# Kernel optimization log

Hardware: AMD Instinct MI355X
Metric: run time of the kernel (lower is better)

Reference implementation:

```python
import jax, jax.numpy as jnp
import numpy as np
from jax import lax

R = 128          # residual channels
DILATION = 4


def setup_inputs() -> dict:
    key = jax.random.key(0)
    ks = jax.random.split(key, 9)
    B, Cin, T = 8, 128, 16000
    Ccond, S, K = 80, 256, 3
    s = 0.05
    return {
        "input": jax.random.normal(ks[0], (B, Cin, T), dtype=jnp.float32),
        "cond_input": jax.random.normal(ks[1], (B, Ccond, T), dtype=jnp.float32),
        "weight_conv": jax.random.normal(ks[2], (2 * R, Cin, K), dtype=jnp.float32) * s,
        "bias_conv": jax.random.normal(ks[3], (2 * R,), dtype=jnp.float32) * s,
        "weight_cond": jax.random.normal(ks[4], (2 * R, Ccond, 1), dtype=jnp.float32) * s,
        "weight_out": jax.random.normal(ks[5], (R, R, 1), dtype=jnp.float32) * s,
        "bias_out": jax.random.normal(ks[6], (R,), dtype=jnp.float32) * s,
        "weight_skip": jax.random.normal(ks[7], (S, R, 1), dtype=jnp.float32) * s,
        "bias_skip": jax.random.normal(ks[8], (S,), dtype=jnp.float32) * s,
    }


def reference(input, cond_input, weight_conv, bias_conv, weight_cond,
              weight_out, bias_out, weight_skip, bias_skip):
    # Causal dilated Conv1d: left-pad (K-1)*dilation
    K = weight_conv.shape[-1]
    pad = (K - 1) * DILATION
    x = lax.conv_general_dilated(
        input, weight_conv, window_strides=(1,),
        padding=[(pad, 0)], rhs_dilation=(DILATION,),
        dimension_numbers=("NCH", "OIH", "NCH"))  # (B, 2R, T)
    x = x + bias_conv[None, :, None]
    # cond_1x1 (kernel 1, no bias), added to pre-activation
    x = x + jnp.einsum("bct,oc->bot", cond_input, weight_cond[:, :, 0])
    # gated activation: tanh(first half) * sigmoid(second half)
    z = jnp.tanh(x[:, :R, :]) * jax.nn.sigmoid(x[:, R:, :])  # (B, R, T)
    skip = jnp.einsum("bct,oc->bot", z, weight_skip[:, :, 0]) + bias_skip[None, :, None]
    output = jnp.einsum("bct,oc->bot", z, weight_out[:, :, 0]) + bias_out[None, :, None]
    return (output, skip)
```

## Files before the change

### kernel.cpp

```cpp
#include <hip/hip_runtime.h>


#define NB 8
#define NT 16000
#define CIN 128
#define CCOND 80
#define CCP 96
#define TT 128
#define NROW 136

typedef __attribute__((ext_vector_type(8))) __bf16 bf16x8;
typedef __attribute__((ext_vector_type(4))) float f32x4;
typedef __attribute__((ext_vector_type(4))) unsigned short u16x4;
typedef __attribute__((ext_vector_type(4))) unsigned int u32x4;

__device__ __forceinline__ unsigned short f2bf(float f) {
  unsigned int u = __float_as_uint(f);
  return (unsigned short)((u + 0x7fffu + ((u >> 16) & 1u)) >> 16);
}
__device__ __forceinline__ bf16x8 ldb8(const unsigned short* p) {
  return *reinterpret_cast<const bf16x8*>(p);
}

__global__ void pack_weights(const float* __restrict__ wc, const float* __restrict__ wcd,
                             const float* __restrict__ wo, const float* __restrict__ wsk,
                             unsigned short* __restrict__ wpc,
                             unsigned short* __restrict__ wpcd,
                             unsigned short* __restrict__ wp2)
{
  int idx = blockIdx.x * 256 + threadIdx.x;
  if (idx < 98304) {
    int o = idx / 384, k = idx - o * 384;
    int tap = k >> 7, c = k & 127;
    wpc[idx] = f2bf(wc[(o * 128 + c) * 3 + tap]);
  } else if (idx < 122880) {
    int i = idx - 98304;
    int o = i / 96, k = i - o * 96;
    wpcd[i] = f2bf(k < CCOND ? wcd[o * CCOND + k] : 0.f);
  } else if (idx < 172032) {
    int i = idx - 122880;
    int m = i >> 7, k = i & 127;
    wp2[i] = f2bf(m < 128 ? wo[m * 128 + k] : wsk[(m - 128) * 128 + k]);
  }
}

__global__ __launch_bounds__(512, 4) void k12_fused(
    const unsigned short* __restrict__ wpc, const unsigned short* __restrict__ wpcd,
    const unsigned short* __restrict__ wp2,
    const float* __restrict__ in, const float* __restrict__ cond,
    const float* __restrict__ bconv, const float* __restrict__ bout,
    const float* __restrict__ bskip, float* __restrict__ out)
{
  __shared__ u32x4 ldsX_[2176];
  __shared__ u32x4 ldsU_[2048];
  char* ldsX = (char*)ldsX_;
  char* ldsU = (char*)ldsU_;

  int b = blockIdx.y;
  int t0 = blockIdx.x * TT;
  int tid = threadIdx.x;
  int lane = tid & 63, w = tid >> 6;
  int l15 = lane & 15, g = lane >> 4;

  #pragma unroll
  for (int rep = 0; rep < 5; ++rep) {
    int gi = rep * 512 + tid;
    if (gi < 16 * NROW) {
      int gch = gi / NROW;
      int row = gi - gch * NROW;
      int t = t0 - 8 + row;
      u32x4 pk = {};
      if (t >= 0) {
        const float* src = &in[((size_t)b * CIN + gch * 8) * NT + t];
        #pragma unroll
        for (int p = 0; p < 4; ++p) {
          float v0 = src[(size_t)(2 * p) * NT];
          float v1 = src[(size_t)(2 * p + 1) * NT];
          pk[p] = (unsigned)f2bf(v0) | ((unsigned)f2bf(v1) << 16);
        }
      }
      *reinterpret_cast<u32x4*>(&ldsX[row * 256 + ((gch ^ (row & 7)) << 4)]) = pk;
    }
  }
  #pragma unroll
  for (int rep = 0; rep < 3; ++rep) {
    int gi = rep * 512 + tid;
    int gch = gi >> 7;
    int row = gi & 127;
    u32x4 pk = {};
    if (gch < 10) {
      const float* src = &cond[((size_t)b * CCOND + gch * 8) * NT + t0 + row];
      #pragma unroll
      for (int p = 0; p < 4; ++p) {
        float v0 = src[(size_t)(2 * p) * NT];
        float v1 = src[(size_t)(2 * p + 1) * NT];
        pk[p] = (unsigned)f2bf(v0) | ((unsigned)f2bf(v1) << 16);
      }
    }
    *reinterpret_cast<u32x4*>(&ldsU[row * 192 + ((gch ^ (row & 3)) << 4)]) = pk;
  }
  __syncthreads();

  int rt = 16 * w + l15, rs = 128 + 16 * w + l15;
  f32x4 at[8] = {}, as_[8] = {};

  #pragma unroll
  for (int gg = 0; gg < 5; ++gg) {
    bf16x8 wt[3], wss[3];
    #pragma unroll
    for (int q = 0; q < 3; ++q) {
      int s = gg * 3 + q;
      if (s < 12) {
        int tap = s >> 2, kc = s & 3;
        wt[q]  = ldb8(&wpc[(size_t)rt * 384 + tap * 128 + kc * 32 + g * 8]);
        wss[q] = ldb8(&wpc[(size_t)rs * 384 + tap * 128 + kc * 32 + g * 8]);
      } else {
        int kc = s - 12;
        wt[q]  = ldb8(&wpcd[(size_t)rt * CCP + kc * 32 + g * 8]);
        wss[q] = ldb8(&wpcd[(size_t)rs * CCP + kc * 32 + g * 8]);
      }
    }
    __builtin_amdgcn_sched_barrier(0);
    #pragma unroll
    for (int q = 0; q < 3; ++q) {
      int s = gg * 3 + q;
      if (s < 12) {
        int tap = s >> 2, kc = s & 3;
        int ck = kc * 4 + g;
        #pragma unroll
        for (int nf = 0; nf < 8; ++nf) {
          int tl = nf * 16 + l15 + tap * 4;
          bf16x8 bfr = *reinterpret_cast<const bf16x8*>(&ldsX[tl * 256 + ((ck ^ (tl & 7)) << 4)]);
          at[nf]  = __builtin_amdgcn_mfma_f32_16x16x32_bf16(wt[q],  bfr, at[nf],  0, 0, 0);
          as_[nf] = __builtin_amdgcn_mfma_f32_16x16x32_bf16(wss[q], bfr, as_[nf], 0, 0, 0);
        }
      } else {
        int kc = s - 12;
        int ck = kc * 4 + g;
        #pragma unroll
        for (int nf = 0; nf < 8; ++nf) {
          int r = nf * 16 + l15;
          bf16x8 bfr = *reinterpret_cast<const bf16x8*>(&ldsU[r * 192 + ((ck ^ (r & 3)) << 4)]);
          at[nf]  = __builtin_amdgcn_mfma_f32_16x16x32_bf16(wt[q],  bfr, at[nf],  0, 0, 0);
          as_[nf] = __builtin_amdgcn_mfma_f32_16x16x32_bf16(wss[q], bfr, as_[nf], 0, 0, 0);
        }
      }
    }
  }

  float btv[4], bsv[4];
  #pragma unroll
  for (int j = 0; j < 4; ++j) {
    btv[j] = bconv[16 * w + g * 4 + j];
    bsv[j] = bconv[128 + 16 * w + g * 4 + j];
  }

  bf16x8 wk2buf[2][4];
  #pragma unroll
  for (int kc = 0; kc < 4; ++kc)
    wk2buf[0][kc] = ldb8(&wp2[(size_t)(48 * w + l15) * 128 + kc * 32 + g * 8]);

  __syncthreads();

  {
    int cg = 2 * w + (g >> 1);
    int off = (g & 1) * 8;
    #pragma unroll
    for (int nf = 0; nf < 8; ++nf) {
      int tl = nf * 16 + l15;
      u16x4 pk;
      #pragma unroll
      for (int j = 0; j < 4; ++j) {
        float a = at[nf][j] + btv[j];
        float s = as_[nf][j] + bsv[j];
        float z = (1.f - 2.f / (1.f + __expf(2.f * a))) * (1.f / (1.f + __expf(-s)));
        pk[j] = f2bf(z);
      }
      *reinterpret_cast<u16x4*>(&ldsU[tl * 256 + ((cg ^ (tl & 7)) << 4) + off]) = pk;
    }
  }
  __syncthreads();

  float* skipp = out + (size_t)NB * 128 * NT;
  #pragma unroll
  for (int mf = 0; mf < 3; ++mf) {
    bf16x8* wcur = wk2buf[mf & 1];
    bf16x8* wnx  = wk2buf[(mf + 1) & 1];
    if (mf < 2) {
      #pragma unroll
      for (int kc = 0; kc < 4; ++kc)
        wnx[kc] = ldb8(&wp2[(size_t)(48 * w + 16 * (mf + 1) + l15) * 128 + kc * 32 + g * 8]);
    }
    __builtin_amdgcn_sched_barrier(0);
    f32x4 am[8] = {};
    #pragma unroll
    for (int kc = 0; kc < 4; ++kc) {
      #pragma unroll
      for (int nf = 0; nf < 8; ++nf) {
        int r = nf * 16 + l15;
        bf16x8 bfr = *reinterpret_cast<const bf16x8*>(&ldsU[r * 256 + (((kc * 4 + g) ^ (r & 7)) << 4)]);
        am[nf] = __builtin_amdgcn_mfma_f32_16x16x32_bf16(wcur[kc], bfr, am[nf], 0, 0, 0);
      }
    }
    int mrow = 48 * w + 16 * mf + g * 4;
    #pragma unroll
    for (int j = 0; j < 4; ++j) {
      int m = mrow + j;
      float bv;
      float* basep;
      if (m < 128) { bv = bout[m];        basep = out   + ((size_t)b * 128 + m) * NT; }
      else         { bv = bskip[m - 128]; basep = skipp + ((size_t)b * 256 + (m - 128)) * NT; }
      #pragma unroll
      for (int nf = 0; nf < 8; ++nf)
        basep[t0 + nf * 16 + l15] = am[nf][j] + bv;
    }
  }
}

extern "C" void kernel_launch(void* const* d_in, const int* in_sizes, int n_in,
                              void* d_out, int out_size, void* d_ws, size_t ws_size,
                              hipStream_t stream)
{
  const float* input = (const float*)d_in[0];
  const float* cond  = (const float*)d_in[1];
  const float* wconv = (const float*)d_in[2];
  const float* bconv = (const float*)d_in[3];
  const float* wcond = (const float*)d_in[4];
  const float* wout  = (const float*)d_in[5];
  const float* boutp = (const float*)d_in[6];
  const float* wskip = (const float*)d_in[7];
  const float* bskip = (const float*)d_in[8];
  float* out = (float*)d_out;

  unsigned short* wpc  = (unsigned short*)d_ws;
  unsigned short* wpcd = wpc + 98304;
  unsigned short* wp2  = wpcd + 24576;

  pack_weights<<<672, 256, 0, stream>>>(wconv, wcond, wout, wskip, wpc, wpcd, wp2);
  k12_fused<<<dim3(NT / TT, NB), 512, 0, stream>>>(wpc, wpcd, wp2, input, cond,
                                                   bconv, boutp, bskip, out);
}
```

Measured before the change: 106.4 us.

## Overlap cond loads with conv MFMAs, use hardware bf16 pack, restructure output GEMM

The input tile is now staged first, followed by a barrier. The cond tile global loads are then issued before the conv-tap MFMAs so they can overlap, and the cond GEMM runs after a second barrier. Float-to-bf16 conversion switches from manual integer rounding to the v_cvt_pk_bf16_f32 instruction. The second GEMM is reorganised into two time halves, each computing all three M fragments with B fragments reused across them, and the weight double-buffer and sched_barriers are dropped. This trades register pressure and an extra barrier for better latency hiding and fewer VALU ops.

```diff
diff --git a/kernel.cpp b/kernel.cpp
--- a/kernel.cpp
+++ b/kernel.cpp
@@ -11,12 +11,17 @@
 
 typedef __attribute__((ext_vector_type(8))) __bf16 bf16x8;
 typedef __attribute__((ext_vector_type(4))) float f32x4;
-typedef __attribute__((ext_vector_type(4))) unsigned short u16x4;
+typedef __attribute__((ext_vector_type(2))) unsigned int u32x2;
 typedef __attribute__((ext_vector_type(4))) unsigned int u32x4;
 
 __device__ __forceinline__ unsigned short f2bf(float f) {
   unsigned int u = __float_as_uint(f);
   return (unsigned short)((u + 0x7fffu + ((u >> 16) & 1u)) >> 16);
+}
+__device__ __forceinline__ unsigned cvtpk(float lo, float hi) {
+  unsigned r;
+  asm("v_cvt_pk_bf16_f32 %0, %1, %2" : "=v"(r) : "v"(lo), "v"(hi));
+  return r;
 }
 __device__ __forceinline__ bf16x8 ldb8(const unsigned short* p) {
   return *reinterpret_cast<const bf16x8*>(p);
@@ -73,15 +78,14 @@
       if (t >= 0) {
         const float* src = &in[((size_t)b * CIN + gch * 8) * NT + t];
         #pragma unroll
-        for (int p = 0; p < 4; ++p) {
-          float v0 = src[(size_t)(2 * p) * NT];
-          float v1 = src[(size_t)(2 * p + 1) * NT];
-          pk[p] = (unsigned)f2bf(v0) | ((unsigned)f2bf(v1) << 16);
-        }
+        for (int p = 0; p < 4; ++p)
+          pk[p] = cvtpk(src[(size_t)(2 * p) * NT], src[(size_t)(2 * p + 1) * NT]);
       }
       *reinterpret_cast<u32x4*>(&ldsX[row * 256 + ((gch ^ (row & 7)) << 4)]) = pk;
     }
   }
+  __syncthreads();
+
   #pragma unroll
   for (int rep = 0; rep < 3; ++rep) {
     int gi = rep * 512 + tid;
@@ -91,59 +95,57 @@
     if (gch < 10) {
       const float* src = &cond[((size_t)b * CCOND + gch * 8) * NT + t0 + row];
       #pragma unroll
-      for (int p = 0; p < 4; ++p) {
-        float v0 = src[(size_t)(2 * p) * NT];
-        float v1 = src[(size_t)(2 * p + 1) * NT];
-        pk[p] = (unsigned)f2bf(v0) | ((unsigned)f2bf(v1) << 16);
-      }
+      for (int p = 0; p < 4; ++p)
+        pk[p] = cvtpk(src[(size_t)(2 * p) * NT], src[(size_t)(2 * p + 1) * NT]);
     }
     *reinterpret_cast<u32x4*>(&ldsU[row * 192 + ((gch ^ (row & 3)) << 4)]) = pk;
   }
-  __syncthreads();
 
   int rt = 16 * w + l15, rs = 128 + 16 * w + l15;
   f32x4 at[8] = {}, as_[8] = {};
 
   #pragma unroll
-  for (int gg = 0; gg < 5; ++gg) {
+  for (int gg = 0; gg < 4; ++gg) {
     bf16x8 wt[3], wss[3];
     #pragma unroll
     for (int q = 0; q < 3; ++q) {
       int s = gg * 3 + q;
-      if (s < 12) {
-        int tap = s >> 2, kc = s & 3;
-        wt[q]  = ldb8(&wpc[(size_t)rt * 384 + tap * 128 + kc * 32 + g * 8]);
-        wss[q] = ldb8(&wpc[(size_t)rs * 384 + tap * 128 + kc * 32 + g * 8]);
-      } else {
-        int kc = s - 12;
-        wt[q]  = ldb8(&wpcd[(size_t)rt * CCP + kc * 32 + g * 8]);
-        wss[q] = ldb8(&wpcd[(size_t)rs * CCP + kc * 32 + g * 8]);
-      }
-    }
-    __builtin_amdgcn_sched_barrier(0);
+      int tap = s >> 2, kc = s & 3;
+      wt[q]  = ldb8(&wpc[(size_t)rt * 384 + tap * 128 + kc * 32 + g * 8]);
+      wss[q] = ldb8(&wpc[(size_t)rs * 384 + tap * 128 + kc * 32 + g * 8]);
+    }
     #pragma unroll
     for (int q = 0; q < 3; ++q) {
       int s = gg * 3 + q;
-      if (s < 12) {
-        int tap = s >> 2, kc = s & 3;
-        int ck = kc * 4 + g;
-        #pragma unroll
-        for (int nf = 0; nf < 8; ++nf) {
-          int tl = nf * 16 + l15 + tap * 4;
-          bf16x8 bfr = *reinterpret_cast<const bf16x8*>(&ldsX[tl * 256 + ((ck ^ (tl & 7)) << 4)]);
-          at[nf]  = __builtin_amdgcn_mfma_f32_16x16x32_bf16(wt[q],  bfr, at[nf],  0, 0, 0);
-          as_[nf] = __builtin_amdgcn_mfma_f32_16x16x32_bf16(wss[q], bfr, as_[nf], 0, 0, 0);
-        }
-      } else {
-        int kc = s - 12;
-        int ck = kc * 4 + g;
-        #pragma unroll
-        for (int nf = 0; nf < 8; ++nf) {
-          int r = nf * 16 + l15;
-          bf16x8 bfr = *reinterpret_cast<const bf16x8*>(&ldsU[r * 192 + ((ck ^ (r & 3)) << 4)]);
-          at[nf]  = __builtin_amdgcn_mfma_f32_16x16x32_bf16(wt[q],  bfr, at[nf],  0, 0, 0);
-          as_[nf] = __builtin_amdgcn_mfma_f32_16x16x32_bf16(wss[q], bfr, as_[nf], 0, 0, 0);
-        }
+      int tap = s >> 2, kc = s & 3;
+      int ck = kc * 4 + g;
+      #pragma unroll
+      for (int nf = 0; nf < 8; ++nf) {
+        int tl = nf * 16 + l15 + tap * 4;
+        bf16x8 bfr = *reinterpret_cast<const bf16x8*>(&ldsX[tl * 256 + ((ck ^ (tl & 7)) << 4)]);
+        at[nf]  = __builtin_amdgcn_mfma_f32_16x16x32_bf16(wt[q],  bfr, at[nf],  0, 0, 0);
+        as_[nf] = __builtin_amdgcn_mfma_f32_16x16x32_bf16(wss[q], bfr, as_[nf], 0, 0, 0);
+      }
+    }
+  }
+  __syncthreads();
+
+  {
+    bf16x8 wt[3], wss[3];
+    #pragma unroll
+    for (int kc = 0; kc < 3; ++kc) {
+      wt[kc]  = ldb8(&wpcd[(size_t)rt * CCP + kc * 32 + g * 8]);
+      wss[kc] = ldb8(&wpcd[(size_t)rs * CCP + kc * 32 + g * 8]);
+    }
+    #pragma unroll
+    for (int kc = 0; kc < 3; ++kc) {
+      int ck = kc * 4 + g;
+      #pragma unroll
+      for (int nf = 0; nf < 8; ++nf) {
+        int r = nf * 16 + l15;
+        bf16x8 bfr = *reinterpret_cast<const bf16x8*>(&ldsU[r * 192 + ((ck ^ (r & 3)) << 4)]);
+        at[nf]  = __builtin_amdgcn_mfma_f32_16x16x32_bf16(wt[kc],  bfr, at[nf],  0, 0, 0);
+        as_[nf] = __builtin_amdgcn_mfma_f32_16x16x32_bf16(wss[kc], bfr, as_[nf], 0, 0, 0);
       }
     }
   }
@@ -154,12 +156,6 @@
     btv[j] = bconv[16 * w + g * 4 + j];
     bsv[j] = bconv[128 + 16 * w + g * 4 + j];
   }
-
-  bf16x8 wk2buf[2][4];
-  #pragma unroll
-  for (int kc = 0; kc < 4; ++kc)
-    wk2buf[0][kc] = ldb8(&wp2[(size_t)(48 * w + l15) * 128 + kc * 32 + g * 8]);
-
   __syncthreads();
 
   {
@@ -168,51 +164,57 @@
     #pragma unroll
     for (int nf = 0; nf < 8; ++nf) {
       int tl = nf * 16 + l15;
-      u16x4 pk;
+      float zv[4];
       #pragma unroll
       for (int j = 0; j < 4; ++j) {
         float a = at[nf][j] + btv[j];
         float s = as_[nf][j] + bsv[j];
-        float z = (1.f - 2.f / (1.f + __expf(2.f * a))) * (1.f / (1.f + __expf(-s)));
-        pk[j] = f2bf(z);
-      }
-      *reinterpret_cast<u16x4*>(&ldsU[tl * 256 + ((cg ^ (tl & 7)) << 4) + off]) = pk;
+        zv[j] = (1.f - 2.f / (1.f + __expf(2.f * a))) * (1.f / (1.f + __expf(-s)));
+      }
+      u32x2 pk;
+      pk[0] = cvtpk(zv[0], zv[1]);
+      pk[1] = cvtpk(zv[2], zv[3]);
+      *reinterpret_cast<u32x2*>(&ldsU[tl * 256 + ((cg ^ (tl & 7)) << 4) + off]) = pk;
     }
   }
   __syncthreads();
 
   float* skipp = out + (size_t)NB * 128 * NT;
   #pragma unroll
-  for (int mf = 0; mf < 3; ++mf) {
-    bf16x8* wcur = wk2buf[mf & 1];
-    bf16x8* wnx  = wk2buf[(mf + 1) & 1];
-    if (mf < 2) {
-      #pragma unroll
-      for (int kc = 0; kc < 4; ++kc)
-        wnx[kc] = ldb8(&wp2[(size_t)(48 * w + 16 * (mf + 1) + l15) * 128 + kc * 32 + g * 8]);
-    }
-    __builtin_amdgcn_sched_barrier(0);
-    f32x4 am[8] = {};
+  for (int half = 0; half < 2; ++half) {
+    f32x4 acc2[3][4] = {};
     #pragma unroll
     for (int kc = 0; kc < 4; ++kc) {
-      #pragma unroll
-      for (int nf = 0; nf < 8; ++nf) {
-        int r = nf * 16 + l15;
-        bf16x8 bfr = *reinterpret_cast<const bf16x8*>(&ldsU[r * 256 + (((kc * 4 + g) ^ (r & 7)) << 4)]);
-        am[nf] = __builtin_amdgcn_mfma_f32_16x16x32_bf16(wcur[kc], bfr, am[nf], 0, 0, 0);
-      }
-    }
-    int mrow = 48 * w + 16 * mf + g * 4;
-    #pragma unroll
-    for (int j = 0; j < 4; ++j) {
-      int m = mrow + j;
-      float bv;
-      float* basep;
-      if (m < 128) { bv = bout[m];        basep = out   + ((size_t)b * 128 + m) * NT; }
-      else         { bv = bskip[m - 128]; basep = skipp + ((size_t)b * 256 + (m - 128)) * NT; }
-      #pragma unroll
-      for (int nf = 0; nf < 8; ++nf)
-        basep[t0 + nf * 16 + l15] = am[nf][j] + bv;
+      bf16x8 w2[3];
+      #pragma unroll
+      for (int mf = 0; mf < 3; ++mf)
+        w2[mf] = ldb8(&wp2[(size_t)(48 * w + 16 * mf + l15) * 128 + kc * 32 + g * 8]);
+      bf16x8 bfr[4];
+      #pragma unroll
+      for (int nf = 0; nf < 4; ++nf) {
+        int r = (half * 4 + nf) * 16 + l15;
+        bfr[nf] = *reinterpret_cast<const bf16x8*>(&ldsU[r * 256 + (((kc * 4 + g) ^ (r & 7)) << 4)]);
+      }
+      #pragma unroll
+      for (int mf = 0; mf < 3; ++mf)
+        #pragma unroll
+        for (int nf = 0; nf < 4; ++nf)
+          acc2[mf][nf] = __builtin_amdgcn_mfma_f32_16x16x32_bf16(w2[mf], bfr[nf], acc2[mf][nf], 0, 0, 0);
+    }
+    #pragma unroll
+    for (int mf = 0; mf < 3; ++mf) {
+      int mrow = 48 * w + 16 * mf + g * 4;
+      #pragma unroll
+      for (int j = 0; j < 4; ++j) {
+        int m = mrow + j;
+        float bv;
+        float* basep;
+        if (m < 128) { bv = bout[m];        basep = out   + ((size_t)b * 128 + m) * NT; }
+        else         { bv = bskip[m - 128]; basep = skipp + ((size_t)b * 256 + (m - 128)) * NT; }
+        #pragma unroll
+        for (int nf = 0; nf < 4; ++nf)
+          basep[t0 + (half * 4 + nf) * 16 + l15] = acc2[mf][nf][j] + bv;
+      }
     }
   }
 }
```

After: 121.1 us. 13.9% more time.

## Shrink time tile to 112 and switch LDS to channel-major layout

Applied to the files above, without the earlier changes.

Reduces the per-block time tile from 128 to 112 columns, which gives 143 blocks per batch with bounds checks for the ragged tail, and replaces the XOR-swizzled row-major LDS layout with a channel-group-major layout using padded strides. The gated activation is written back into the input LDS buffer rather than a separate one, so shared memory per block drops and more blocks can be resident or the grid fills the CUs more evenly. The risk is LDS bank conflicts from the new unswizzled strides, extra boundary branches, and a smaller MFMA N-tile per wave.

```diff
diff --git a/kernel.cpp b/kernel.cpp
--- a/kernel.cpp
+++ b/kernel.cpp
@@ -5,9 +5,11 @@
 #define NT 16000
 #define CIN 128
 #define CCOND 80
-#define CCP 96
-#define TT 128
-#define NROW 136
+#define TT 112
+#define XR 120
+#define XSTRIDE 1920
+#define CSTRIDE 1792
+#define NBLK 143
 
 typedef __attribute__((ext_vector_type(8))) __bf16 bf16x8;
 typedef __attribute__((ext_vector_type(4))) float f32x4;
@@ -51,10 +53,10 @@
     const float* __restrict__ bconv, const float* __restrict__ bout,
     const float* __restrict__ bskip, float* __restrict__ out)
 {
-  __shared__ u32x4 ldsX_[2176];
-  __shared__ u32x4 ldsU_[2048];
+  __shared__ u32x4 ldsX_[XR * 16];
+  __shared__ u32x4 ldsC_[112 * 10];
   char* ldsX = (char*)ldsX_;
-  char* ldsU = (char*)ldsU_;
+  char* ldsC = (char*)ldsC_;
 
   int b = blockIdx.y;
   int t0 = blockIdx.x * TT;
@@ -63,14 +65,14 @@
   int l15 = lane & 15, g = lane >> 4;
 
   #pragma unroll
-  for (int rep = 0; rep < 5; ++rep) {
+  for (int rep = 0; rep < 4; ++rep) {
     int gi = rep * 512 + tid;
-    if (gi < 16 * NROW) {
-      int gch = gi / NROW;
-      int row = gi - gch * NROW;
+    if (gi < 16 * XR) {
+      int gch = gi / XR;
+      int row = gi - gch * XR;
       int t = t0 - 8 + row;
       u32x4 pk = {};
-      if (t >= 0) {
+      if (t >= 0 && t < NT) {
         const float* src = &in[((size_t)b * CIN + gch * 8) * NT + t];
         #pragma unroll
         for (int p = 0; p < 4; ++p) {
@@ -79,30 +81,33 @@
           pk[p] = (unsigned)f2bf(v0) | ((unsigned)f2bf(v1) << 16);
         }
       }
-      *reinterpret_cast<u32x4*>(&ldsX[row * 256 + ((gch ^ (row & 7)) << 4)]) = pk;
+      *reinterpret_cast<u32x4*>(&ldsX[gch * XSTRIDE + row * 16]) = pk;
     }
   }
   #pragma unroll
   for (int rep = 0; rep < 3; ++rep) {
     int gi = rep * 512 + tid;
-    int gch = gi >> 7;
-    int row = gi & 127;
-    u32x4 pk = {};
-    if (gch < 10) {
-      const float* src = &cond[((size_t)b * CCOND + gch * 8) * NT + t0 + row];
-      #pragma unroll
-      for (int p = 0; p < 4; ++p) {
-        float v0 = src[(size_t)(2 * p) * NT];
-        float v1 = src[(size_t)(2 * p + 1) * NT];
-        pk[p] = (unsigned)f2bf(v0) | ((unsigned)f2bf(v1) << 16);
-      }
-    }
-    *reinterpret_cast<u32x4*>(&ldsU[row * 192 + ((gch ^ (row & 3)) << 4)]) = pk;
+    if (gi < 10 * TT) {
+      int gch = gi / TT;
+      int row = gi - gch * TT;
+      int t = t0 + row;
+      u32x4 pk = {};
+      if (t < NT) {
+        const float* src = &cond[((size_t)b * CCOND + gch * 8) * NT + t];
+        #pragma unroll
+        for (int p = 0; p < 4; ++p) {
+          float v0 = src[(size_t)(2 * p) * NT];
+          float v1 = src[(size_t)(2 * p + 1) * NT];
+          pk[p] = (unsigned)f2bf(v0) | ((unsigned)f2bf(v1) << 16);
+        }
+      }
+      *reinterpret_cast<u32x4*>(&ldsC[gch * CSTRIDE + row * 16]) = pk;
+    }
   }
   __syncthreads();
 
   int rt = 16 * w + l15, rs = 128 + 16 * w + l15;
-  f32x4 at[8] = {}, as_[8] = {};
+  f32x4 at[7] = {}, as_[7] = {};
 
   #pragma unroll
   for (int gg = 0; gg < 5; ++gg) {
@@ -116,8 +121,8 @@
         wss[q] = ldb8(&wpc[(size_t)rs * 384 + tap * 128 + kc * 32 + g * 8]);
       } else {
         int kc = s - 12;
-        wt[q]  = ldb8(&wpcd[(size_t)rt * CCP + kc * 32 + g * 8]);
-        wss[q] = ldb8(&wpcd[(size_t)rs * CCP + kc * 32 + g * 8]);
+        wt[q]  = ldb8(&wpcd[(size_t)rt * 96 + kc * 32 + g * 8]);
+        wss[q] = ldb8(&wpcd[(size_t)rs * 96 + kc * 32 + g * 8]);
       }
     }
     __builtin_amdgcn_sched_barrier(0);
@@ -128,9 +133,9 @@
         int tap = s >> 2, kc = s & 3;
         int ck = kc * 4 + g;
         #pragma unroll
-        for (int nf = 0; nf < 8; ++nf) {
-          int tl = nf * 16 + l15 + tap * 4;
-          bf16x8 bfr = *reinterpret_cast<const bf16x8*>(&ldsX[tl * 256 + ((ck ^ (tl & 7)) << 4)]);
+        for (int nf = 0; nf < 7; ++nf) {
+          int row = nf * 16 + l15 + tap * 4;
+          bf16x8 bfr = *reinterpret_cast<const bf16x8*>(&ldsX[ck * XSTRIDE + row * 16]);
           at[nf]  = __builtin_amdgcn_mfma_f32_16x16x32_bf16(wt[q],  bfr, at[nf],  0, 0, 0);
           as_[nf] = __builtin_amdgcn_mfma_f32_16x16x32_bf16(wss[q], bfr, as_[nf], 0, 0, 0);
         }
@@ -138,9 +143,10 @@
         int kc = s - 12;
         int ck = kc * 4 + g;
         #pragma unroll
-        for (int nf = 0; nf < 8; ++nf) {
+        for (int nf = 0; nf < 7; ++nf) {
           int r = nf * 16 + l15;
-          bf16x8 bfr = *reinterpret_cast<const bf16x8*>(&ldsU[r * 192 + ((ck ^ (r & 3)) << 4)]);
+          bf16x8 bfr = {};
+          if (ck < 10) bfr = *reinterpret_cast<const bf16x8*>(&ldsC[ck * CSTRIDE + r * 16]);
           at[nf]  = __builtin_amdgcn_mfma_f32_16x16x32_bf16(wt[q],  bfr, at[nf],  0, 0, 0);
           as_[nf] = __builtin_amdgcn_mfma_f32_16x16x32_bf16(wss[q], bfr, as_[nf], 0, 0, 0);
         }
@@ -166,7 +172,7 @@
     int cg = 2 * w + (g >> 1);
     int off = (g & 1) * 8;
     #pragma unroll
-    for (int nf = 0; nf < 8; ++nf) {
+    for (int nf = 0; nf < 7; ++nf) {
       int tl = nf * 16 + l15;
       u16x4 pk;
       #pragma unroll
@@ -176,7 +182,7 @@
         float z = (1.f - 2.f / (1.f + __expf(2.f * a))) * (1.f / (1.f + __expf(-s)));
         pk[j] = f2bf(z);
       }
-      *reinterpret_cast<u16x4*>(&ldsU[tl * 256 + ((cg ^ (tl & 7)) << 4) + off]) = pk;
+      *reinterpret_cast<u16x4*>(&ldsX[cg * XSTRIDE + tl * 16 + off]) = pk;
     }
   }
   __syncthreads();
@@ -192,13 +198,14 @@
         wnx[kc] = ldb8(&wp2[(size_t)(48 * w + 16 * (mf + 1) + l15) * 128 + kc * 32 + g * 8]);
     }
     __builtin_amdgcn_sched_barrier(0);
-    f32x4 am[8] = {};
+    f32x4 am[7] = {};
     #pragma unroll
     for (int kc = 0; kc < 4; ++kc) {
-      #pragma unroll
-      for (int nf = 0; nf < 8; ++nf) {
+      int gk = kc * 4 + g;
+      #pragma unroll
+      for (int nf = 0; nf < 7; ++nf) {
         int r = nf * 16 + l15;
-        bf16x8 bfr = *reinterpret_cast<const bf16x8*>(&ldsU[r * 256 + (((kc * 4 + g) ^ (r & 7)) << 4)]);
+        bf16x8 bfr = *reinterpret_cast<const bf16x8*>(&ldsX[gk * XSTRIDE + r * 16]);
         am[nf] = __builtin_amdgcn_mfma_f32_16x16x32_bf16(wcur[kc], bfr, am[nf], 0, 0, 0);
       }
     }
@@ -211,8 +218,10 @@
       if (m < 128) { bv = bout[m];        basep = out   + ((size_t)b * 128 + m) * NT; }
       else         { bv = bskip[m - 128]; basep = skipp + ((size_t)b * 256 + (m - 128)) * NT; }
       #pragma unroll
-      for (int nf = 0; nf < 8; ++nf)
-        basep[t0 + nf * 16 + l15] = am[nf][j] + bv;
+      for (int nf = 0; nf < 7; ++nf) {
+        int t = t0 + nf * 16 + l15;
+        if (t < NT) basep[t] = am[nf][j] + bv;
+      }
     }
   }
 }
@@ -237,6 +246,6 @@
   unsigned short* wp2  = wpcd + 24576;
 
   pack_weights<<<672, 256, 0, stream>>>(wconv, wcond, wout, wskip, wpc, wpcd, wp2);
-  k12_fused<<<dim3(NT / TT, NB), 512, 0, stream>>>(wpc, wpcd, wp2, input, cond,
-                                                   bconv, boutp, bskip, out);
-}
+  k12_fused<<<dim3(NBLK, NB), 512, 0, stream>>>(wpc, wpcd, wp2, input, cond,
+                                                bconv, boutp, bskip, out);
+}
```

New measurement: 128.9 us. +21.2%, slower.
